# Performance work log

Measured on AMD Instinct MI355X. Metric: run time of the kernel, lower is better.

Reference implementation:

```python
import jax, jax.numpy as jnp
import numpy as np

B, N, DIN, DOUT, DA = 8, 2048, 128, 128, 2
NEG_SLOPE = 0.2


def setup_inputs() -> dict:
    key = jax.random.key(0)
    k = jax.random.split(key, 7)
    x = jax.random.normal(k[0], (B, N, DIN), dtype=jnp.float32)
    mask = jax.random.randint(k[1], (B, N, N), 0, 2, dtype=jnp.int32)
    s = 1.0 / np.sqrt(DIN)
    Wr = jax.random.uniform(k[2], (DA, DIN), jnp.float32, -s, s)      # linear_row.weight
    Wc = jax.random.uniform(k[3], (DA, DIN), jnp.float32, -s, s)      # linear_col.weight
    sa = 1.0 / np.sqrt(2 * DA)
    Wcat = jax.random.uniform(k[4], (2 * DA,), jnp.float32, -sa, sa)  # linear_concat.weight [1, 2*DA] flattened
    Wx = jax.random.uniform(k[5], (DOUT, DIN), jnp.float32, -s, s)    # linear_x.weight
    bx = jax.random.uniform(k[6], (DOUT,), jnp.float32, -s, s)        # linear_x.bias
    return {"x": x, "mask": mask, "Wr": Wr, "Wc": Wc, "Wcat": Wcat, "Wx": Wx, "bx": bx}


def reference(x, mask, Wr, Wc, Wcat, Wx, bx):
    # Row/col projections to tiny attention dim: [B, N, DA]
    row = jnp.einsum('bnd,ad->bna', x, Wr)
    col = jnp.einsum('bnd,ad->bna', x, Wc)
    # Concat scoring: e_ij = linear_concat(LeakyReLU(cat(row_i, col_j)))
    # decomposes as a1 . LR(row_i) + a2 . LR(col_j) -- avoids materializing [B,N,N,2*DA]
    a1, a2 = Wcat[:DA], Wcat[DA:]
    lr_row = jax.nn.leaky_relu(row, NEG_SLOPE) @ a1   # [B, N]
    lr_col = jax.nn.leaky_relu(col, NEG_SLOPE) @ a2   # [B, N]
    e = lr_row[:, :, None] + lr_col[:, None, :]       # [B, N, N]
    # Masked softmax over columns j
    e = jnp.where(mask > 0, e, jnp.float32(-1e9))
    atten = jax.nn.softmax(e, axis=-1)                # [B, N, N]
    # Value projection + combine
    xv = jnp.einsum('bnd,od->bno', x, Wx) + bx        # [B, N, DOUT]
    out = jnp.einsum('bij,bjo->bio', atten, xv)       # [B, N, DOUT]
    return out
```

## Files before the change

### kernel.cpp

```cpp
#include <hip/hip_runtime.h>


typedef __bf16 bf16x8 __attribute__((ext_vector_type(8)));
typedef float  f32x4  __attribute__((ext_vector_type(4)));
typedef int    i32x4  __attribute__((ext_vector_type(4)));
typedef unsigned int u32;

#define MFMA_BF16(a, b, c) __builtin_amdgcn_mfma_f32_16x16x32_bf16((a), (b), (c), 0, 0, 0)

#define GLOAD_LDS16(gp, lp)                                                     \
  __builtin_amdgcn_global_load_lds(                                             \
      (const __attribute__((address_space(1))) void*)(gp),                      \
      (__attribute__((address_space(3))) void*)(lp), 16, 0, 0)

static __device__ __forceinline__ bf16x8 cvt8(f32x4 a, f32x4 b) {
  bf16x8 r;
  r[0] = (__bf16)a[0]; r[1] = (__bf16)a[1]; r[2] = (__bf16)a[2]; r[3] = (__bf16)a[3];
  r[4] = (__bf16)b[0]; r[5] = (__bf16)b[1]; r[6] = (__bf16)b[2]; r[7] = (__bf16)b[3];
  return r;
}

__global__ __launch_bounds__(256) void prep_kernel(
    const float* __restrict__ x, const float* __restrict__ Wc,
    const float* __restrict__ Wcat, const float* __restrict__ Wx,
    const float* __restrict__ bx, __bf16* __restrict__ u)
{
  __shared__ __bf16 lds[9216];
  const int blk = blockIdx.x;
  const int b = blk >> 5, mt = blk & 31;
  const int wv = threadIdx.x >> 6, lane = threadIdx.x & 63;
  const int np = lane & 15, G = lane >> 4;
  const int r0 = mt * 64 + wv * 16;

  const float* xp = x + ((size_t)(b * 2048 + r0 + np)) * 128 + G * 8;
  bf16x8 af[4];
#pragma unroll
  for (int kk = 0; kk < 4; ++kk) {
    f32x4 x0 = *(const f32x4*)(xp + kk * 32);
    f32x4 x1 = *(const f32x4*)(xp + kk * 32 + 4);
    af[kk] = cvt8(x0, x1);
  }

  f32x4 acc[8], accC;
#pragma unroll
  for (int n = 0; n < 8; ++n) { acc[n][0] = 0.f; acc[n][1] = 0.f; acc[n][2] = 0.f; acc[n][3] = 0.f; }
  accC[0] = accC[1] = accC[2] = accC[3] = 0.f;

#pragma unroll
  for (int n = 0; n < 8; ++n) {
    const float* wp = Wx + (n * 16 + np) * 128 + G * 8;
#pragma unroll
    for (int kk = 0; kk < 4; ++kk) {
      f32x4 w0 = *(const f32x4*)(wp + kk * 32);
      f32x4 w1 = *(const f32x4*)(wp + kk * 32 + 4);
      acc[n] = MFMA_BF16(af[kk], cvt8(w0, w1), acc[n]);
    }
  }
#pragma unroll
  for (int kk = 0; kk < 4; ++kk) {
    bf16x8 bf;
    if (np < 2) {
      const float* cp = Wc + np * 128 + kk * 32 + G * 8;
      f32x4 c0 = *(const f32x4*)cp;
      f32x4 c1 = *(const f32x4*)(cp + 4);
      bf = cvt8(c0, c1);
    } else {
#pragma unroll
      for (int j = 0; j < 8; ++j) bf[j] = (__bf16)0.0f;
    }
    accC = MFMA_BF16(af[kk], bf, accC);
  }

  const float a20 = Wcat[2], a21 = Wcat[3];
  float wexp[4];
#pragma unroll
  for (int r = 0; r < 4; ++r) {
    float c0 = __shfl(accC[r], lane & 48);
    float c1 = __shfl(accC[r], (lane & 48) | 1);
    c0 = c0 > 0.f ? c0 : 0.2f * c0;
    c1 = c1 > 0.f ? c1 : 0.2f * c1;
    wexp[r] = __expf(c0 * a20 + c1 * a21);
  }

  const int t_rel = wv >> 1;
  const int g_store = (wv & 1) * 2 + (G >> 1);
  const int j0 = (G & 1) * 4;
#pragma unroll
  for (int n = 0; n < 8; ++n) {
    float bxv = bx[n * 16 + np];
    __bf16 v[4];
#pragma unroll
    for (int r = 0; r < 4; ++r) v[r] = (__bf16)(wexp[r] * (acc[n][r] + bxv));
    *(__bf16*)&lds[(t_rel * 9 + n) * 512 + g_store * 128 + np * 8 + j0 + 0] = v[0];
    lds[(t_rel * 9 + n) * 512 + g_store * 128 + np * 8 + j0 + 1] = v[1];
    lds[(t_rel * 9 + n) * 512 + g_store * 128 + np * 8 + j0 + 2] = v[2];
    lds[(t_rel * 9 + n) * 512 + g_store * 128 + np * 8 + j0 + 3] = v[3];
  }
  {
#pragma unroll
    for (int r = 0; r < 4; ++r)
      lds[(t_rel * 9 + 8) * 512 + g_store * 128 + np * 8 + j0 + r] =
          (np == 0) ? (__bf16)wexp[r] : (__bf16)0.0f;
  }
  __syncthreads();
  __bf16* dst = u + ((size_t)(b * 64 + mt * 2)) * 9 * 512;
  for (int s = threadIdx.x; s < 1152; s += 256)
    ((i32x4*)dst)[s] = ((const i32x4*)lds)[s];
}

__global__ __launch_bounds__(256) void packA_kernel(
    const int* __restrict__ mask, __bf16* __restrict__ Abuf)
{
  __shared__ int sm[32 * 129];
  const int b = blockIdx.x & 7, rt = blockIdx.x >> 3;
  const int tid = threadIdx.x;
  const int* mbase = mask + ((size_t)b * 2048 + rt * 32) * 2048;
  __bf16* obase = Abuf + (size_t)(b * 64 + rt) * 64 * 1024;

  const int row_r = tid >> 3;
  const int cb8 = (tid & 7) * 16;
  const int f = tid >> 5;
  const int tk = f >> 1, mi = f & 1;

  for (int ch = 0; ch < 16; ++ch) {
    const int* rp = mbase + (size_t)row_r * 2048 + ch * 128 + cb8;
    i32x4 v0 = *(const i32x4*)rp;
    i32x4 v1 = *(const i32x4*)(rp + 4);
    i32x4 v2 = *(const i32x4*)(rp + 8);
    i32x4 v3 = *(const i32x4*)(rp + 12);
    __syncthreads();
    *(i32x4*)&sm[row_r * 129 + cb8 + 0]  = v0;
    *(i32x4*)&sm[row_r * 129 + cb8 + 4]  = v1;
    *(i32x4*)&sm[row_r * 129 + cb8 + 8]  = v2;
    *(i32x4*)&sm[row_r * 129 + cb8 + 12] = v3;
    __syncthreads();
#pragma unroll
    for (int h = 0; h < 2; ++h) {
      const int l = (tid & 31) + h * 32;
      const int row = mi * 16 + (l & 15);
      const int col = tk * 32 + (l >> 4) * 8;
      u32 P[4];
#pragma unroll
      for (int q = 0; q < 4; ++q) {
        u32 lo = sm[row * 129 + col + 2 * q]     ? 0x3F80u : 0u;
        u32 hi = sm[row * 129 + col + 2 * q + 1] ? 0x3F800000u : 0u;
        P[q] = lo | hi;
      }
      __bf16* op = obase + ((size_t)(ch * 4 + tk) * 2 + mi) * 512 + l * 8;
      *(i32x4*)op = *(const i32x4*)P;
    }
  }
}

__global__ __launch_bounds__(256) void attn_kernel(
    const __bf16* __restrict__ Abuf, const __bf16* __restrict__ u,
    float* __restrict__ out)
{
  __shared__ char smem[4 * 11264];
  const int b = blockIdx.x & 7, rt = blockIdx.x >> 3;
  const int wv = threadIdx.x >> 6, lane = threadIdx.x & 63;
  const int np = lane & 15, G = lane >> 4;
  const int row0 = rt * 32;
  const int n0 = wv * 2, n1 = n0 + 1;

  const char* gA = (const char*)Abuf + (size_t)(b * 64 + rt) * 64 * 2048;
  const char* gu = (const char*)u + (size_t)b * 64 * 9216;

  f32x4 acc[2][3];
#pragma unroll
  for (int mi = 0; mi < 2; ++mi)
#pragma unroll
    for (int n = 0; n < 3; ++n) { acc[mi][n][0] = 0.f; acc[mi][n][1] = 0.f; acc[mi][n][2] = 0.f; acc[mi][n][3] = 0.f; }

#define STAGE(it, nb)                                                          \
  do {                                                                         \
    char* dst = smem + (nb) * 11264;                                           \
    if (wv == 0) {                                                             \
      const char* ga = gA + (size_t)(it) * 2048 + lane * 16;                   \
      GLOAD_LDS16(ga, dst);                                                    \
      GLOAD_LDS16(ga + 1024, dst + 1024);                                      \
      GLOAD_LDS16(gu + (size_t)(it) * 9216 + lane * 16, dst + 2048);           \
    } else if (wv == 3) {                                                      \
      const char* gp = gu + (size_t)(it) * 9216 + 7 * 1024 + lane * 16;        \
      GLOAD_LDS16(gp, dst + 2048 + 7 * 1024);                                  \
      GLOAD_LDS16(gp + 1024, dst + 2048 + 8 * 1024);                           \
    } else {                                                                   \
      const char* gp = gu + (size_t)(it) * 9216 + (wv * 3 - 2) * 1024 + lane * 16; \
      GLOAD_LDS16(gp, dst + 2048 + (wv * 3 - 2) * 1024);                       \
      GLOAD_LDS16(gp + 1024, dst + 2048 + (wv * 3 - 1) * 1024);                \
      GLOAD_LDS16(gp + 2048, dst + 2048 + (wv * 3) * 1024);                    \
    }                                                                          \
  } while (0)

#define CONSUME(nb)                                                            \
  do {                                                                         \
    const char* buf = smem + (nb) * 11264;                                     \
    bf16x8 A0 = *(const bf16x8*)(buf + lane * 16);                             \
    bf16x8 A1 = *(const bf16x8*)(buf + 1024 + lane * 16);                      \
    const char* ub = buf + 2048;                                               \
    bf16x8 U0 = *(const bf16x8*)(ub + n0 * 1024 + lane * 16);                  \
    bf16x8 U1 = *(const bf16x8*)(ub + n1 * 1024 + lane * 16);                  \
    bf16x8 UD = *(const bf16x8*)(ub + 8 * 1024 + lane * 16);                   \
    acc[0][0] = MFMA_BF16(A0, U0, acc[0][0]);                                  \
    acc[0][1] = MFMA_BF16(A0, U1, acc[0][1]);                                  \
    acc[0][2] = MFMA_BF16(A0, UD, acc[0][2]);                                  \
    acc[1][0] = MFMA_BF16(A1, U0, acc[1][0]);                                  \
    acc[1][1] = MFMA_BF16(A1, U1, acc[1][1]);                                  \
    acc[1][2] = MFMA_BF16(A1, UD, acc[1][2]);                                  \
  } while (0)

  STAGE(0, 0); STAGE(1, 1); STAGE(2, 2);
  const int wvu = __builtin_amdgcn_readfirstlane(wv);

  for (int it = 0; it <= 61; ++it) {
    if (wvu == 3) asm volatile("s_waitcnt vmcnt(4)" ::: "memory");
    else          asm volatile("s_waitcnt vmcnt(6)" ::: "memory");
    __builtin_amdgcn_s_barrier();
    CONSUME(it & 3);
    if (it <= 60) STAGE(it + 3, (it + 3) & 3);
  }
  if (wvu == 3) asm volatile("s_waitcnt vmcnt(2)" ::: "memory");
  else          asm volatile("s_waitcnt vmcnt(3)" ::: "memory");
  __builtin_amdgcn_s_barrier();
  CONSUME(62 & 3);
  asm volatile("s_waitcnt vmcnt(0)" ::: "memory");
  __builtin_amdgcn_s_barrier();
  CONSUME(63 & 3);
#undef STAGE
#undef CONSUME

#pragma unroll
  for (int mi = 0; mi < 2; ++mi) {
#pragma unroll
    for (int r = 0; r < 4; ++r) {
      float den = __shfl(acc[mi][2][r], lane & 48);
      float inv = 1.0f / den;
      float* op = out + ((size_t)b * 2048 + row0 + mi * 16 + 4 * G + r) * 128 + np;
      op[n0 * 16] = acc[mi][0][r] * inv;
      op[n1 * 16] = acc[mi][1][r] * inv;
    }
  }
}

extern "C" void kernel_launch(void* const* d_in, const int* in_sizes, int n_in,
                              void* d_out, int out_size, void* d_ws, size_t ws_size,
                              hipStream_t stream) {
  const float* x    = (const float*)d_in[0];
  const int*   mask = (const int*)d_in[1];
  const float* Wc   = (const float*)d_in[3];
  const float* Wcat = (const float*)d_in[4];
  const float* Wx   = (const float*)d_in[5];
  const float* bx   = (const float*)d_in[6];
  float* out = (float*)d_out;

  const size_t U_BYTES = (size_t)8 * 64 * 9 * 512 * 2;
  const size_t A_BYTES = (size_t)8 * 2048 * 2048 * 2;
  if (ws_size < U_BYTES + A_BYTES) return;
  __bf16* u    = (__bf16*)d_ws;
  __bf16* Abuf = (__bf16*)((char*)d_ws + U_BYTES);

  prep_kernel<<<256, 256, 0, stream>>>(x, Wc, Wcat, Wx, bx, u);
  packA_kernel<<<512, 256, 0, stream>>>(mask, Abuf);
  attn_kernel<<<512, 256, 0, stream>>>(Abuf, u, out);
}
```

Before: 251.3 us.

## Replace LDS-staged pipeline with direct register double-buffered global loads in attn kernel

The attention kernel no longer stages A and u tiles through LDS with global_load_lds, a 4-deep ring, waitcnt and barriers. Each wave now loads its MFMA operands straight from global memory into two register sets and alternates compute and load. This removes the LDS round trip and the per-iteration barriers, at the cost of redundant global loads: all four waves now fetch the same A and UD tiles, and the prefetch depth is shallower. The prep kernel's bf16 store loop is also tidied up.

```diff
diff --git a/kernel.cpp b/kernel.cpp
--- a/kernel.cpp
+++ b/kernel.cpp
@@ -7,11 +7,6 @@
 typedef unsigned int u32;
 
 #define MFMA_BF16(a, b, c) __builtin_amdgcn_mfma_f32_16x16x32_bf16((a), (b), (c), 0, 0, 0)
-
-#define GLOAD_LDS16(gp, lp)                                                     \
-  __builtin_amdgcn_global_load_lds(                                             \
-      (const __attribute__((address_space(1))) void*)(gp),                      \
-      (__attribute__((address_space(3))) void*)(lp), 16, 0, 0)
 
 static __device__ __forceinline__ bf16x8 cvt8(f32x4 a, f32x4 b) {
   bf16x8 r;
@@ -88,13 +83,10 @@
 #pragma unroll
   for (int n = 0; n < 8; ++n) {
     float bxv = bx[n * 16 + np];
-    __bf16 v[4];
-#pragma unroll
-    for (int r = 0; r < 4; ++r) v[r] = (__bf16)(wexp[r] * (acc[n][r] + bxv));
-    *(__bf16*)&lds[(t_rel * 9 + n) * 512 + g_store * 128 + np * 8 + j0 + 0] = v[0];
-    lds[(t_rel * 9 + n) * 512 + g_store * 128 + np * 8 + j0 + 1] = v[1];
-    lds[(t_rel * 9 + n) * 512 + g_store * 128 + np * 8 + j0 + 2] = v[2];
-    lds[(t_rel * 9 + n) * 512 + g_store * 128 + np * 8 + j0 + 3] = v[3];
+#pragma unroll
+    for (int r = 0; r < 4; ++r)
+      lds[(t_rel * 9 + n) * 512 + g_store * 128 + np * 8 + j0 + r] =
+          (__bf16)(wexp[r] * (acc[n][r] + bxv));
   }
   {
 #pragma unroll
@@ -156,15 +148,14 @@
     const __bf16* __restrict__ Abuf, const __bf16* __restrict__ u,
     float* __restrict__ out)
 {
-  __shared__ char smem[4 * 11264];
   const int b = blockIdx.x & 7, rt = blockIdx.x >> 3;
   const int wv = threadIdx.x >> 6, lane = threadIdx.x & 63;
   const int np = lane & 15, G = lane >> 4;
   const int row0 = rt * 32;
   const int n0 = wv * 2, n1 = n0 + 1;
 
-  const char* gA = (const char*)Abuf + (size_t)(b * 64 + rt) * 64 * 2048;
-  const char* gu = (const char*)u + (size_t)b * 64 * 9216;
+  const char* gA = (const char*)Abuf + (size_t)(b * 64 + rt) * 64 * 2048 + lane * 16;
+  const char* gu = (const char*)u + (size_t)b * 64 * 9216 + lane * 16;
 
   f32x4 acc[2][3];
 #pragma unroll
@@ -172,62 +163,40 @@
 #pragma unroll
     for (int n = 0; n < 3; ++n) { acc[mi][n][0] = 0.f; acc[mi][n][1] = 0.f; acc[mi][n][2] = 0.f; acc[mi][n][3] = 0.f; }
 
-#define STAGE(it, nb)                                                          \
-  do {                                                                         \
-    char* dst = smem + (nb) * 11264;                                           \
-    if (wv == 0) {                                                             \
-      const char* ga = gA + (size_t)(it) * 2048 + lane * 16;                   \
-      GLOAD_LDS16(ga, dst);                                                    \
-      GLOAD_LDS16(ga + 1024, dst + 1024);                                      \
-      GLOAD_LDS16(gu + (size_t)(it) * 9216 + lane * 16, dst + 2048);           \
-    } else if (wv == 3) {                                                      \
-      const char* gp = gu + (size_t)(it) * 9216 + 7 * 1024 + lane * 16;        \
-      GLOAD_LDS16(gp, dst + 2048 + 7 * 1024);                                  \
-      GLOAD_LDS16(gp + 1024, dst + 2048 + 8 * 1024);                           \
-    } else {                                                                   \
-      const char* gp = gu + (size_t)(it) * 9216 + (wv * 3 - 2) * 1024 + lane * 16; \
-      GLOAD_LDS16(gp, dst + 2048 + (wv * 3 - 2) * 1024);                       \
-      GLOAD_LDS16(gp + 1024, dst + 2048 + (wv * 3 - 1) * 1024);                \
-      GLOAD_LDS16(gp + 2048, dst + 2048 + (wv * 3) * 1024);                    \
-    }                                                                          \
+  bf16x8 A0X, A1X, U0X, U1X, UDX;
+  bf16x8 A0Y, A1Y, U0Y, U1Y, UDY;
+
+#define LOADF(S, t)                                                      \
+  do {                                                                   \
+    const char* ga_ = gA + (size_t)(t) * 2048;                           \
+    const char* gu_ = gu + (size_t)(t) * 9216;                           \
+    A0##S = *(const bf16x8*)(ga_);                                       \
+    A1##S = *(const bf16x8*)(ga_ + 1024);                                \
+    U0##S = *(const bf16x8*)(gu_ + n0 * 1024);                           \
+    U1##S = *(const bf16x8*)(gu_ + n1 * 1024);                           \
+    UD##S = *(const bf16x8*)(gu_ + 8 * 1024);                            \
   } while (0)
 
-#define CONSUME(nb)                                                            \
-  do {                                                                         \
-    const char* buf = smem + (nb) * 11264;                                     \
-    bf16x8 A0 = *(const bf16x8*)(buf + lane * 16);                             \
-    bf16x8 A1 = *(const bf16x8*)(buf + 1024 + lane * 16);                      \
-    const char* ub = buf + 2048;                                               \
-    bf16x8 U0 = *(const bf16x8*)(ub + n0 * 1024 + lane * 16);                  \
-    bf16x8 U1 = *(const bf16x8*)(ub + n1 * 1024 + lane * 16);                  \
-    bf16x8 UD = *(const bf16x8*)(ub + 8 * 1024 + lane * 16);                   \
-    acc[0][0] = MFMA_BF16(A0, U0, acc[0][0]);                                  \
-    acc[0][1] = MFMA_BF16(A0, U1, acc[0][1]);                                  \
-    acc[0][2] = MFMA_BF16(A0, UD, acc[0][2]);                                  \
-    acc[1][0] = MFMA_BF16(A1, U0, acc[1][0]);                                  \
-    acc[1][1] = MFMA_BF16(A1, U1, acc[1][1]);                                  \
-    acc[1][2] = MFMA_BF16(A1, UD, acc[1][2]);                                  \
+#define COMPF(S)                                                         \
+  do {                                                                   \
+    acc[0][0] = MFMA_BF16(A0##S, U0##S, acc[0][0]);                      \
+    acc[0][1] = MFMA_BF16(A0##S, U1##S, acc[0][1]);                      \
+    acc[0][2] = MFMA_BF16(A0##S, UD##S, acc[0][2]);                      \
+    acc[1][0] = MFMA_BF16(A1##S, U0##S, acc[1][0]);                      \
+    acc[1][1] = MFMA_BF16(A1##S, U1##S, acc[1][1]);                      \
+    acc[1][2] = MFMA_BF16(A1##S, UD##S, acc[1][2]);                      \
   } while (0)
 
-  STAGE(0, 0); STAGE(1, 1); STAGE(2, 2);
-  const int wvu = __builtin_amdgcn_readfirstlane(wv);
-
-  for (int it = 0; it <= 61; ++it) {
-    if (wvu == 3) asm volatile("s_waitcnt vmcnt(4)" ::: "memory");
-    else          asm volatile("s_waitcnt vmcnt(6)" ::: "memory");
-    __builtin_amdgcn_s_barrier();
-    CONSUME(it & 3);
-    if (it <= 60) STAGE(it + 3, (it + 3) & 3);
-  }
-  if (wvu == 3) asm volatile("s_waitcnt vmcnt(2)" ::: "memory");
-  else          asm volatile("s_waitcnt vmcnt(3)" ::: "memory");
-  __builtin_amdgcn_s_barrier();
-  CONSUME(62 & 3);
-  asm volatile("s_waitcnt vmcnt(0)" ::: "memory");
-  __builtin_amdgcn_s_barrier();
-  CONSUME(63 & 3);
-#undef STAGE
-#undef CONSUME
+  LOADF(X, 0);
+  LOADF(Y, 1);
+  for (int t = 0; t < 62; t += 2) {
+    COMPF(X); LOADF(X, t + 2);
+    COMPF(Y); LOADF(Y, t + 3);
+  }
+  COMPF(X);
+  COMPF(Y);
+#undef LOADF
+#undef COMPF
 
 #pragma unroll
   for (int mi = 0; mi < 2; ++mi) {
```

Measured after the change: 252.4 us. Within noise of the previous version (+0.4%).
